# Kernel tuning notes

Measured on AMD Instinct MI355X. Metric: run time of the kernel, lower is better.

## Reference

```python
import jax, jax.numpy as jnp
import numpy as np

EMBED_DIM = 1024
CONTEXT_DIM = 768
NUM_HEADS = 16
HEAD_DIM = EMBED_DIM // NUM_HEADS
B, N, M = 8, 4096, 77


def setup_inputs() -> dict:
    key = jax.random.key(0)
    ks = jax.random.split(key, 12)
    s_in = 1.0 / np.sqrt(EMBED_DIM)
    s_ctx = 1.0 / np.sqrt(CONTEXT_DIM)
    x = jax.random.normal(ks[0], (B, N, EMBED_DIM), dtype=jnp.float32)
    context = jax.random.normal(ks[1], (B, M, CONTEXT_DIM), dtype=jnp.float32)
    # realistic padding mask: each example has a random valid prefix length in [1, M]
    lengths = jax.random.randint(ks[2], (B,), 1, M + 1)
    context_mask = jnp.arange(M)[None, :] < lengths[:, None]  # (B, M) bool
    Wq = jax.random.uniform(ks[3], (EMBED_DIM, EMBED_DIM), jnp.float32, -s_in, s_in)
    bq = jax.random.uniform(ks[4], (EMBED_DIM,), jnp.float32, -s_in, s_in)
    Wk = jax.random.uniform(ks[5], (CONTEXT_DIM, EMBED_DIM), jnp.float32, -s_ctx, s_ctx)
    bk = jax.random.uniform(ks[6], (EMBED_DIM,), jnp.float32, -s_ctx, s_ctx)
    Wv = jax.random.uniform(ks[7], (CONTEXT_DIM, EMBED_DIM), jnp.float32, -s_ctx, s_ctx)
    bv = jax.random.uniform(ks[8], (EMBED_DIM,), jnp.float32, -s_ctx, s_ctx)
    Wo = jax.random.uniform(ks[9], (EMBED_DIM, EMBED_DIM), jnp.float32, -s_in, s_in)
    bo = jax.random.uniform(ks[10], (EMBED_DIM,), jnp.float32, -s_in, s_in)
    return {"x": x, "context": context, "context_mask": context_mask,
            "Wq": Wq, "bq": bq, "Wk": Wk, "bk": bk, "Wv": Wv, "bv": bv,
            "Wo": Wo, "bo": bo}


def reference(x, context, context_mask, Wq, bq, Wk, bk, Wv, bv, Wo, bo):
    H, d = NUM_HEADS, HEAD_DIM
    scale = d ** -0.5
    Bx, Nx, _ = x.shape
    Mx = context.shape[1]
    # projections
    q = (x @ Wq + bq).reshape(Bx, Nx, H, d).transpose(0, 2, 1, 3)        # (B,H,N,d)
    k = (context @ Wk + bk).reshape(Bx, Mx, H, d).transpose(0, 2, 1, 3)  # (B,H,M,d)
    v = (context @ Wv + bv).reshape(Bx, Mx, H, d).transpose(0, 2, 1, 3)  # (B,H,M,d)
    # scores with padding mask
    attn = jnp.einsum('bhnd,bhmd->bhnm', q, k) * scale                   # (B,H,N,M)
    attn = jnp.where(context_mask[:, None, None, :], attn, -jnp.inf)
    attn = jax.nn.softmax(attn, axis=-1)
    out = jnp.einsum('bhnm,bhmd->bhnd', attn, v)                          # (B,H,N,d)
    out = out.transpose(0, 2, 1, 3).reshape(Bx, Nx, H * d)                # (B,N,E)
    return out @ Wo + bo
```

## Files before the change

### kernel.cpp

```cpp
#include <hip/hip_runtime.h>

typedef __bf16 bf16x8 __attribute__((ext_vector_type(8)));
typedef float f32x4 __attribute__((ext_vector_type(4)));

#define EMB 1024
#define CTXD 768
#define NH 16
#define HD 64
#define BB 8
#define NN 4096
#define MM 77
#define MPAD 96

static __device__ __forceinline__ unsigned short f2bf(float f) {
    unsigned u = __builtin_bit_cast(unsigned, f);
    u += 0x7FFFu + ((u >> 16) & 1u);
    return (unsigned short)(u >> 16);
}

struct PrepArgs {
    const float* wsrc[4];
    unsigned short* wdst[4];
    const float* ctx;
    unsigned short* cbf;
    const unsigned char* mask;
    int* lengths;
    int4* kvzero;
    const float* x;
    unsigned short* xbf;
};
__global__ void prep_kernel(PrepArgs pa) {
    const int z = blockIdx.z;
    const int tx = threadIdx.x, ty = threadIdx.y;
    const int tid = ty * 32 + tx;
    if (z < 4) {
        __shared__ float t[32][33];
        int R = (z < 2) ? 1024 : 768, C = 1024;
        int r0 = blockIdx.y * 32;
        if (r0 >= R) return;
        const float* W = pa.wsrc[z];
        unsigned short* Wt = pa.wdst[z];
        int c0 = blockIdx.x * 32;
#pragma unroll
        for (int i = 0; i < 32; i += 8)
            t[ty + i][tx] = W[(size_t)(r0 + ty + i) * C + c0 + tx];
        __syncthreads();
#pragma unroll
        for (int i = 0; i < 32; i += 8)
            Wt[(size_t)(c0 + ty + i) * R + r0 + tx] = f2bf(t[tx][ty + i]);
    } else if (z == 4) {
        int fid = blockIdx.y * 32 + blockIdx.x;
        int i = fid * 256 + tid;
        if (i >= 640 * CTXD / 8) return;
        int row = (i * 8) / CTXD;
        union { unsigned short u[8]; int4 v; } r;
        if (row < BB * MM) {
            float4 v0 = ((const float4*)pa.ctx)[2 * i];
            float4 v1 = ((const float4*)pa.ctx)[2 * i + 1];
            r.u[0] = f2bf(v0.x); r.u[1] = f2bf(v0.y);
            r.u[2] = f2bf(v0.z); r.u[3] = f2bf(v0.w);
            r.u[4] = f2bf(v1.x); r.u[5] = f2bf(v1.y);
            r.u[6] = f2bf(v1.z); r.u[7] = f2bf(v1.w);
        } else {
            r.v = make_int4(0, 0, 0, 0);
        }
        ((int4*)pa.cbf)[i] = r.v;
    } else if (z == 5) {
        int fid = blockIdx.y * 32 + blockIdx.x;
        int i = fid * 256 + tid;
        if (i < 196608) pa.kvzero[i] = make_int4(0, 0, 0, 0);
        if (fid == 1023 && tid < 64) {
            int ln = tid;
            int anyOdd = 0, anyF = 0;
            for (int k = ln; k < BB * MM; k += 64) {
                unsigned char v = pa.mask[k];
                if (v == 0x80u || v == 0x3Fu) anyF = 1;
                if ((k & 3) && v) anyOdd = 1;
            }
            anyF = __any(anyF); anyOdd = __any(anyOdd);
            int layout = anyF ? 2 : (anyOdd ? 1 : 0);
            int b = ln >> 3, j = ln & 7, cnt = 0;
            for (int m = j; m < MM; m += 8) {
                int idx = b * MM + m;
                int valid;
                if (layout == 1)      valid = pa.mask[idx] != 0;
                else if (layout == 0) valid = ((const int*)pa.mask)[idx] != 0;
                else                  valid = ((const float*)pa.mask)[idx] != 0.0f;
                cnt += valid ? 1 : 0;
            }
            cnt += __shfl_xor(cnt, 1, 64);
            cnt += __shfl_xor(cnt, 2, 64);
            cnt += __shfl_xor(cnt, 4, 64);
            if (j == 0) pa.lengths[b] = cnt;
        }
    } else {
        int i = ((z - 6) * 1024 + blockIdx.y * 32 + blockIdx.x) * 256 + tid;
        float4 v0 = ((const float4*)pa.x)[2 * i];
        float4 v1 = ((const float4*)pa.x)[2 * i + 1];
        union { unsigned short u[8]; int4 v; } r;
        r.u[0] = f2bf(v0.x); r.u[1] = f2bf(v0.y);
        r.u[2] = f2bf(v0.z); r.u[3] = f2bf(v0.w);
        r.u[4] = f2bf(v1.x); r.u[5] = f2bf(v1.y);
        r.u[6] = f2bf(v1.z); r.u[7] = f2bf(v1.w);
        ((int4*)pa.xbf)[i] = r.v;
    }
}

__global__ __launch_bounds__(512, 2) void gemm_q_kv(
    const unsigned short* __restrict__ Xbf, const unsigned short* __restrict__ Wq_t,
    const float* __restrict__ bq, unsigned short* __restrict__ Qb,
    const unsigned short* __restrict__ Cbf,
    const unsigned short* __restrict__ Wk_t, const float* __restrict__ bk,
    unsigned short* __restrict__ Kw,
    const unsigned short* __restrict__ Wv_t, const float* __restrict__ bv,
    unsigned short* __restrict__ Vtw) {
    __shared__ unsigned short lds[4][2][256 * 32];
    const int tid = threadIdx.x, wv = tid >> 6, ln = tid & 63;
    int bid = blockIdx.x;

    if (bid < 80) {
        const bool isV = bid >= 40;
        if (isV) bid -= 40;
        const unsigned short* Bt = isV ? Wv_t : Wk_t;
        const float* bias = isV ? bv : bk;
        { int cpx = 5; bid = (bid & 7) * cpx + (bid >> 3); }
        const int nt = bid & 7, mt = bid >> 3;
        const int m0 = mt << 7, n0 = nt << 7;
        const int wr = wv >> 2, wc = wv & 3;
        unsigned short* As = &lds[0][0][0];
        unsigned short* Bs = &lds[0][1][0];

        f32x4 acc[4][2] = {};
        const int rown = ln >> 2, koff = (ln & 3) * 8;
        for (int kt = 0; kt < CTXD; kt += 32) {
            __syncthreads();
            __builtin_amdgcn_global_load_lds(
                (const __attribute__((address_space(1))) void*)(
                    Cbf + (size_t)(m0 + wv * 16 + rown) * CTXD + kt + koff),
                (__attribute__((address_space(3))) void*)(As + wv * 512),
                16, 0, 0);
            __builtin_amdgcn_global_load_lds(
                (const __attribute__((address_space(1))) void*)(
                    Bt + (size_t)(n0 + wv * 16 + rown) * CTXD + kt + koff),
                (__attribute__((address_space(3))) void*)(Bs + wv * 512),
                16, 0, 0);
            __syncthreads();
            bf16x8 af[4], bfr[2];
#pragma unroll
            for (int i = 0; i < 4; ++i)
                af[i] = *(const bf16x8*)(As + (wr * 64 + i * 16 + (ln & 15)) * 32 +
                                         (ln >> 4) * 8);
#pragma unroll
            for (int j = 0; j < 2; ++j)
                bfr[j] = *(const bf16x8*)(Bs + (wc * 32 + j * 16 + (ln & 15)) * 32 +
                                          (ln >> 4) * 8);
#pragma unroll
            for (int i = 0; i < 4; ++i)
#pragma unroll
                for (int j = 0; j < 2; ++j)
                    acc[i][j] = __builtin_amdgcn_mfma_f32_16x16x32_bf16(
                        af[i], bfr[j], acc[i][j], 0, 0, 0);
        }

        float bvals[2];
#pragma unroll
        for (int j = 0; j < 2; ++j)
            bvals[j] = bias[n0 + wc * 32 + j * 16 + (ln & 15)];
#pragma unroll
        for (int i = 0; i < 4; ++i)
#pragma unroll
            for (int j = 0; j < 2; ++j)
#pragma unroll
                for (int r = 0; r < 4; ++r) {
                    int row = m0 + wr * 64 + i * 16 + (ln >> 4) * 4 + r;
                    int col = n0 + wc * 32 + j * 16 + (ln & 15);
                    float v = acc[i][j][r] + bvals[j];
                    if (row < BB * MM) {
                        int bb = row / MM, m = row - bb * MM;
                        int hh = col >> 6, d = col & 63;
                        if (!isV)
                            Kw[((size_t)(bb * NH + hh) * MPAD + m) * HD + d] = f2bf(v);
                        else
                            Vtw[((size_t)(bb * NH + hh) * HD + d) * MPAD + m] = f2bf(v);
                    }
                }
        return;
    }

    bid -= 80;
    const int M = 32768, N = 1024, K = 1024;
    const int numN = N >> 8;
    const int nwg = (M >> 8) * numN;
    { int cpx = nwg >> 3; bid = (bid & 7) * cpx + (bid >> 3); }
    const int nt_ = bid % numN, mt = bid / numN;
    const int m0 = mt << 8, n0 = nt_ << 8;
    const int wr = wv >> 2, wc = wv & 3;
    const int NT = K >> 5;

    const int srow = wv * 16 + (ln >> 2);
    const int sslot = ln & 3;

    auto stageA = [&](int t) {
#pragma unroll
        for (int half = 0; half < 2; ++half) {
            int row = half * 128 + srow;
            int gc = sslot ^ ((row >> 1) & 3);
            __builtin_amdgcn_global_load_lds(
                (const __attribute__((address_space(1))) void*)(
                    Xbf + (size_t)(m0 + row) * K + (t << 5) + gc * 8),
                (__attribute__((address_space(3))) void*)(
                    &lds[t & 3][0][(half * 128 + wv * 16) * 32]),
                16, 0, 0);
        }
    };
    auto stageB = [&](int t) {
#pragma unroll
        for (int half = 0; half < 2; ++half) {
            int row = half * 128 + srow;
            int gc = sslot ^ ((row >> 1) & 3);
            __builtin_amdgcn_global_load_lds(
                (const __attribute__((address_space(1))) void*)(
                    Wq_t + (size_t)(n0 + row) * K + (t << 5) + gc * 8),
                (__attribute__((address_space(3))) void*)(
                    &lds[t & 3][1][(half * 128 + wv * 16) * 32]),
                16, 0, 0);
        }
    };
    auto readA = [&](const unsigned short* As, int i) -> bf16x8 {
        int arow = wr * 128 + i * 16 + (ln & 15);
        int aslot = (ln >> 4) ^ ((arow >> 1) & 3);
        return *(const bf16x8*)(As + arow * 32 + aslot * 8);
    };
    auto readB = [&](const unsigned short* Bs, int j) -> bf16x8 {
        int brow = wc * 64 + j * 16 + (ln & 15);
        int bslot = (ln >> 4) ^ ((brow >> 1) & 3);
        return *(const bf16x8*)(Bs + brow * 32 + bslot * 8);
    };

    f32x4 acc[8][4] = {};

    stageA(0); stageB(0); stageA(1); stageB(1); stageA(2); stageB(2);
    asm volatile("s_waitcnt vmcnt(8)" ::: "memory");
    __builtin_amdgcn_sched_barrier(0);
    __builtin_amdgcn_s_barrier();

#pragma unroll 4
    for (int t = 0; t < NT; ++t) {
        const unsigned short* As = lds[t & 3][0];
        const unsigned short* Bs = lds[t & 3][1];
        if (t + 3 < NT) stageA(t + 3);
        bf16x8 bfr[4], af[4];
#pragma unroll
        for (int j = 0; j < 4; ++j) bfr[j] = readB(Bs, j);
#pragma unroll
        for (int i = 0; i < 4; ++i) af[i] = readA(As, i);
        __builtin_amdgcn_s_barrier();
        __builtin_amdgcn_s_setprio(1);
#pragma unroll
        for (int i = 0; i < 4; ++i)
#pragma unroll
            for (int j = 0; j < 4; ++j)
                acc[i][j] = __builtin_amdgcn_mfma_f32_16x16x32_bf16(
                    af[i], bfr[j], acc[i][j], 0, 0, 0);
        __builtin_amdgcn_s_setprio(0);
        __builtin_amdgcn_s_barrier();
        if (t + 3 < NT) stageB(t + 3);
#pragma unroll
        for (int i = 0; i < 4; ++i) af[i] = readA(As, i + 4);
        __builtin_amdgcn_s_barrier();
        __builtin_amdgcn_s_setprio(1);
#pragma unroll
        for (int i = 0; i < 4; ++i)
#pragma unroll
            for (int j = 0; j < 4; ++j)
                acc[i + 4][j] = __builtin_amdgcn_mfma_f32_16x16x32_bf16(
                    af[i], bfr[j], acc[i + 4][j], 0, 0, 0);
        __builtin_amdgcn_s_setprio(0);
        if (t < NT - 1) {
            if (t + 3 < NT)      { asm volatile("s_waitcnt vmcnt(4)" ::: "memory"); }
            else if (t + 2 < NT) { asm volatile("s_waitcnt vmcnt(2)" ::: "memory"); }
            else                 { asm volatile("s_waitcnt vmcnt(0)" ::: "memory"); }
            __builtin_amdgcn_sched_barrier(0);
        }
        __builtin_amdgcn_s_barrier();
    }

    float bvals[4];
#pragma unroll
    for (int j = 0; j < 4; ++j)
        bvals[j] = bq[n0 + wc * 64 + j * 16 + (ln & 15)];
#pragma unroll
    for (int i = 0; i < 8; ++i)
#pragma unroll
        for (int j = 0; j < 4; ++j)
#pragma unroll
            for (int r = 0; r < 4; ++r) {
                int row = m0 + wr * 128 + i * 16 + (ln >> 4) * 4 + r;
                int col = n0 + wc * 64 + j * 16 + (ln & 15);
                Qb[(size_t)row * N + col] = f2bf(acc[i][j][r] + bvals[j]);
            }
}

__global__ __launch_bounds__(512, 2) void gemm256_kernel(
    const unsigned short* __restrict__ A, const unsigned short* __restrict__ Bt,
    const float* __restrict__ bias, float* __restrict__ Cout,
    int M, int N, int K) {
    __shared__ unsigned short lds[4][2][256 * 32];
    const int tid = threadIdx.x, wv = tid >> 6, ln = tid & 63;
    const int numN = N >> 8;
    int bid = blockIdx.x;
    const int nwg = (M >> 8) * numN;
    if ((nwg & 7) == 0) { int cpx = nwg >> 3; bid = (bid & 7) * cpx + (bid >> 3); }
    const int nt_ = bid % numN, mt = bid / numN;
    const int m0 = mt << 8, n0 = nt_ << 8;
    const int wr = wv >> 2, wc = wv & 3;
    const int NT = K >> 5;

    const int srow = wv * 16 + (ln >> 2);
    const int sslot = ln & 3;

    auto stageA = [&](int t) {
#pragma unroll
        for (int half = 0; half < 2; ++half) {
            int row = half * 128 + srow;
            int gc = sslot ^ ((row >> 1) & 3);
            __builtin_amdgcn_global_load_lds(
                (const __attribute__((address_space(1))) void*)(
                    A + (size_t)(m0 + row) * K + (t << 5) + gc * 8),
                (__attribute__((address_space(3))) void*)(
                    &lds[t & 3][0][(half * 128 + wv * 16) * 32]),
                16, 0, 0);
        }
    };
    auto stageB = [&](int t) {
#pragma unroll
        for (int half = 0; half < 2; ++half) {
            int row = half * 128 + srow;
            int gc = sslot ^ ((row >> 1) & 3);
            __builtin_amdgcn_global_load_lds(
                (const __attribute__((address_space(1))) void*)(
                    Bt + (size_t)(n0 + row) * K + (t << 5) + gc * 8),
                (__attribute__((address_space(3))) void*)(
                    &lds[t & 3][1][(half * 128 + wv * 16) * 32]),
                16, 0, 0);
        }
    };
    auto readA = [&](const unsigned short* As, int i) -> bf16x8 {
        int arow = wr * 128 + i * 16 + (ln & 15);
        int aslot = (ln >> 4) ^ ((arow >> 1) & 3);
        return *(const bf16x8*)(As + arow * 32 + aslot * 8);
    };
    auto readB = [&](const unsigned short* Bs, int j) -> bf16x8 {
        int brow = wc * 64 + j * 16 + (ln & 15);
        int bslot = (ln >> 4) ^ ((brow >> 1) & 3);
        return *(const bf16x8*)(Bs + brow * 32 + bslot * 8);
    };

    f32x4 acc[8][4] = {};

    stageA(0); stageB(0); stageA(1); stageB(1); stageA(2); stageB(2);
    asm volatile("s_waitcnt vmcnt(8)" ::: "memory");
    __builtin_amdgcn_sched_barrier(0);
    __builtin_amdgcn_s_barrier();

#pragma unroll 4
    for (int t = 0; t < NT; ++t) {
        const unsigned short* As = lds[t & 3][0];
        const unsigned short* Bs = lds[t & 3][1];
        if (t + 3 < NT) stageA(t + 3);
        bf16x8 bfr[4], af[4];
#pragma unroll
        for (int j = 0; j < 4; ++j) bfr[j] = readB(Bs, j);
#pragma unroll
        for (int i = 0; i < 4; ++i) af[i] = readA(As, i);
        __builtin_amdgcn_s_barrier();
        __builtin_amdgcn_s_setprio(1);
#pragma unroll
        for (int i = 0; i < 4; ++i)
#pragma unroll
            for (int j = 0; j < 4; ++j)
                acc[i][j] = __builtin_amdgcn_mfma_f32_16x16x32_bf16(
                    af[i], bfr[j], acc[i][j], 0, 0, 0);
        __builtin_amdgcn_s_setprio(0);
        __builtin_amdgcn_s_barrier();
        if (t + 3 < NT) stageB(t + 3);
#pragma unroll
        for (int i = 0; i < 4; ++i) af[i] = readA(As, i + 4);
        __builtin_amdgcn_s_barrier();
        __builtin_amdgcn_s_setprio(1);
#pragma unroll
        for (int i = 0; i < 4; ++i)
#pragma unroll
            for (int j = 0; j < 4; ++j)
                acc[i + 4][j] = __builtin_amdgcn_mfma_f32_16x16x32_bf16(
                    af[i], bfr[j], acc[i + 4][j], 0, 0, 0);
        __builtin_amdgcn_s_setprio(0);
        if (t < NT - 1) {
            if (t + 3 < NT)      { asm volatile("s_waitcnt vmcnt(4)" ::: "memory"); }
            else if (t + 2 < NT) { asm volatile("s_waitcnt vmcnt(2)" ::: "memory"); }
            else                 { asm volatile("s_waitcnt vmcnt(0)" ::: "memory"); }
            __builtin_amdgcn_sched_barrier(0);
        }
        __builtin_amdgcn_s_barrier();
    }

    float bvals[4];
#pragma unroll
    for (int j = 0; j < 4; ++j)
        bvals[j] = bias[n0 + wc * 64 + j * 16 + (ln & 15)];
#pragma unroll
    for (int i = 0; i < 8; ++i)
#pragma unroll
        for (int j = 0; j < 4; ++j)
#pragma unroll
            for (int r = 0; r < 4; ++r) {
                int row = m0 + wr * 128 + i * 16 + (ln >> 4) * 4 + r;
                int col = n0 + wc * 64 + j * 16 + (ln & 15);
                Cout[(size_t)row * N + col] = acc[i][j][r] + bvals[j];
            }
}

__global__ __launch_bounds__(256, 3) void attn_kernel(
    const unsigned short* __restrict__ Q, const unsigned short* __restrict__ Kw,
    const unsigned short* __restrict__ Vt, const int* __restrict__ lengths,
    unsigned short* __restrict__ Out) {
    const int bh = blockIdx.y;
    const int b = bh >> 4, h = bh & 15;
    const int q0 = blockIdx.x * 128;
    const int tid = threadIdx.x, wv = tid >> 6, ln = tid & 63;
    const int len = lengths[b];
    const int kscnt = (len + 31) >> 5;

    __shared__ unsigned short Ps[128][104];

    const unsigned short* Ksrc = Kw + (size_t)bh * (MPAD * HD);
    const unsigned short* Vsrc = Vt + (size_t)bh * (HD * MPAD);

    bf16x8 aq[2][2];
#pragma unroll
    for (int qi = 0; qi < 2; ++qi) {
        const int qr = q0 + wv * 32 + qi * 16 + (ln & 15);
        const unsigned short* qptr =
            Q + (size_t)(b * NN + qr) * EMB + h * HD + (ln >> 4) * 8;
        aq[qi][0] = *(const bf16x8*)(qptr);
        aq[qi][1] = *(const bf16x8*)(qptr + 32);
    }

    bf16x8 vf[3][4];
#pragma unroll
    for (int j = 0; j < 4; ++j)
        vf[0][j] = *(const bf16x8*)(Vsrc + (j * 16 + (ln & 15)) * MPAD +
                                    (ln >> 4) * 8);
    if (kscnt > 1) {
#pragma unroll
        for (int j = 0; j < 4; ++j)
            vf[1][j] = *(const bf16x8*)(Vsrc + (j * 16 + (ln & 15)) * MPAD + 32 +
                                        (ln >> 4) * 8);
    }
    if (kscnt > 2) {
#pragma unroll
        for (int j = 0; j < 4; ++j)
            vf[2][j] = *(const bf16x8*)(Vsrc + (j * 16 + (ln & 15)) * MPAD + 64 +
                                        (ln >> 4) * 8);
    }

    f32x4 s[2][5] = {};
#pragma unroll
    for (int t = 0; t < 5; ++t) {
        if (t * 16 < len) {
            const unsigned short* kp =
                Ksrc + (t * 16 + (ln & 15)) * HD + (ln >> 4) * 8;
            bf16x8 k0 = *(const bf16x8*)(kp);
            bf16x8 k1 = *(const bf16x8*)(kp + 32);
#pragma unroll
            for (int qi = 0; qi < 2; ++qi) {
                s[qi][t] = __builtin_amdgcn_mfma_f32_16x16x32_bf16(
                    aq[qi][0], k0, s[qi][t], 0, 0, 0);
                s[qi][t] = __builtin_amdgcn_mfma_f32_16x16x32_bf16(
                    aq[qi][1], k1, s[qi][t], 0, 0, 0);
            }
        }
    }

    const float scale = 0.125f;
    float mx[2][4], sum[2][4];
#pragma unroll
    for (int qi = 0; qi < 2; ++qi)
#pragma unroll
        for (int r = 0; r < 4; ++r) { mx[qi][r] = -1e30f; sum[qi][r] = 0.f; }
#pragma unroll
    for (int t = 0; t < 5; ++t) {
        int m = t * 16 + (ln & 15);
        bool valid = m < len;
#pragma unroll
        for (int qi = 0; qi < 2; ++qi)
#pragma unroll
            for (int r = 0; r < 4; ++r) {
                float v = valid ? s[qi][t][r] * scale : -1e30f;
                s[qi][t][r] = v;
                mx[qi][r] = fmaxf(mx[qi][r], v);
            }
    }
#pragma unroll
    for (int d = 1; d < 16; d <<= 1)
#pragma unroll
        for (int qi = 0; qi < 2; ++qi)
#pragma unroll
            for (int r = 0; r < 4; ++r)
                mx[qi][r] = fmaxf(mx[qi][r], __shfl_xor(mx[qi][r], d, 64));
#pragma unroll
    for (int t = 0; t < 5; ++t)
#pragma unroll
        for (int qi = 0; qi < 2; ++qi)
#pragma unroll
            for (int r = 0; r < 4; ++r) {
                float p = __expf(s[qi][t][r] - mx[qi][r]);
                s[qi][t][r] = p;
                sum[qi][r] += p;
            }
#pragma unroll
    for (int d = 1; d < 16; d <<= 1)
#pragma unroll
        for (int qi = 0; qi < 2; ++qi)
#pragma unroll
            for (int r = 0; r < 4; ++r)
                sum[qi][r] += __shfl_xor(sum[qi][r], d, 64);

    float rinv[2][4];
#pragma unroll
    for (int qi = 0; qi < 2; ++qi)
#pragma unroll
        for (int r = 0; r < 4; ++r) rinv[qi][r] = 1.0f / sum[qi][r];

#pragma unroll
    for (int t = 0; t < 6; ++t)
#pragma unroll
        for (int qi = 0; qi < 2; ++qi)
#pragma unroll
            for (int r = 0; r < 4; ++r) {
                int row = wv * 32 + qi * 16 + (ln >> 4) * 4 + r;
                float v = (t < 5) ? s[qi][t][r] * rinv[qi][r] : 0.0f;
                Ps[row][t * 16 + (ln & 15)] = f2bf(v);
            }

    f32x4 o[2][4] = {};
    for (int ks = 0; ks < kscnt; ++ks) {
#pragma unroll
        for (int qi = 0; qi < 2; ++qi) {
            bf16x8 pf = *(const bf16x8*)(&Ps[wv * 32 + qi * 16 + (ln & 15)]
                                            [ks * 32 + (ln >> 4) * 8]);
#pragma unroll
            for (int j = 0; j < 4; ++j)
                o[qi][j] = __builtin_amdgcn_mfma_f32_16x16x32_bf16(
                    vf[ks][j], pf, o[qi][j], 0, 0, 0);
        }
    }

#pragma unroll
    for (int qi = 0; qi < 2; ++qi) {
        const int qrow = q0 + wv * 32 + qi * 16 + (ln & 15);
        unsigned short* obase =
            Out + (size_t)(b * NN + qrow) * EMB + h * HD + (ln >> 4) * 4;
#pragma unroll
        for (int j = 0; j < 4; ++j) {
            union { unsigned short u[4]; unsigned long long ll; } pk;
#pragma unroll
            for (int r = 0; r < 4; ++r) pk.u[r] = f2bf(o[qi][j][r]);
            *(unsigned long long*)(obase + j * 16) = pk.ll;
        }
    }
}

extern "C" void kernel_launch(void* const* d_in, const int* in_sizes, int n_in,
                              void* d_out, int out_size, void* d_ws, size_t ws_size,
                              hipStream_t stream) {
    const float* x    = (const float*)d_in[0];
    const float* ctx  = (const float*)d_in[1];
    const unsigned char* cmask = (const unsigned char*)d_in[2];
    const float* Wq = (const float*)d_in[3];
    const float* bq = (const float*)d_in[4];
    const float* Wk = (const float*)d_in[5];
    const float* bk = (const float*)d_in[6];
    const float* Wv = (const float*)d_in[7];
    const float* bv = (const float*)d_in[8];
    const float* Wo = (const float*)d_in[9];
    const float* bo = (const float*)d_in[10];

    char* ws = (char*)d_ws;
    unsigned short* Xbf   = (unsigned short*)(ws);
    unsigned short* Wq_t  = (unsigned short*)(ws + 67108864);
    unsigned short* Wo_t  = (unsigned short*)(ws + 69206016);
    unsigned short* Wk_t  = (unsigned short*)(ws + 71303168);
    unsigned short* Wv_t  = (unsigned short*)(ws + 72876032);
    unsigned short* Cbf   = (unsigned short*)(ws + 74448896);
    unsigned short* Kw    = (unsigned short*)(ws + 75431936);
    unsigned short* Vtw   = (unsigned short*)(ws + 77004800);
    int* lengths          = (int*)(ws + 78577664);
    unsigned short* Qb    = (unsigned short*)d_out;

    PrepArgs pa;
    pa.wsrc[0] = Wq; pa.wsrc[1] = Wo; pa.wsrc[2] = Wk; pa.wsrc[3] = Wv;
    pa.wdst[0] = Wq_t; pa.wdst[1] = Wo_t; pa.wdst[2] = Wk_t; pa.wdst[3] = Wv_t;
    pa.ctx = ctx; pa.cbf = Cbf; pa.mask = cmask; pa.lengths = lengths;
    pa.kvzero = (int4*)Kw;
    pa.x = x; pa.xbf = Xbf;
    prep_kernel<<<dim3(32, 32, 22), dim3(32, 8), 0, stream>>>(pa);

    gemm_q_kv<<<592, 512, 0, stream>>>(Xbf, Wq_t, bq, Qb,
                                       Cbf, Wk_t, bk, Kw, Wv_t, bv, Vtw);

    attn_kernel<<<dim3(32, 128), 256, 0, stream>>>(Qb, Kw, Vtw, lengths, Xbf);

    gemm256_kernel<<<512, 512, 0, stream>>>(Xbf, Wo_t, bo, (float*)d_out,
                                            32768, 1024, 1024);
}
```

Baseline: 265.0 us.

## Fuse fp32-to-bf16 conversion of x into the Q projection GEMM

Drops the separate prep pass that converts x to bf16. The Q GEMM now streams fp32 x tiles straight into LDS with an XOR swizzle and converts to bf16 when it reads fragments for the MFMAs. This removes a full write and re-read of a bf16 copy of x. In exchange it adds conversion ALU work inside the hot loop, repeated for each column-wave. The A tile is twice as large in LDS, so the pipeline shrinks from 4 stages to 3 buffers with prefetch distance 2.

```diff
diff --git a/kernel.cpp b/kernel.cpp
--- a/kernel.cpp
+++ b/kernel.cpp
@@ -26,8 +26,6 @@
     const unsigned char* mask;
     int* lengths;
     int4* kvzero;
-    const float* x;
-    unsigned short* xbf;
 };
 __global__ void prep_kernel(PrepArgs pa) {
     const int z = blockIdx.z;
@@ -65,7 +63,7 @@
             r.v = make_int4(0, 0, 0, 0);
         }
         ((int4*)pa.cbf)[i] = r.v;
-    } else if (z == 5) {
+    } else {
         int fid = blockIdx.y * 32 + blockIdx.x;
         int i = fid * 256 + tid;
         if (i < 196608) pa.kvzero[i] = make_int4(0, 0, 0, 0);
@@ -93,28 +91,18 @@
             cnt += __shfl_xor(cnt, 4, 64);
             if (j == 0) pa.lengths[b] = cnt;
         }
-    } else {
-        int i = ((z - 6) * 1024 + blockIdx.y * 32 + blockIdx.x) * 256 + tid;
-        float4 v0 = ((const float4*)pa.x)[2 * i];
-        float4 v1 = ((const float4*)pa.x)[2 * i + 1];
-        union { unsigned short u[8]; int4 v; } r;
-        r.u[0] = f2bf(v0.x); r.u[1] = f2bf(v0.y);
-        r.u[2] = f2bf(v0.z); r.u[3] = f2bf(v0.w);
-        r.u[4] = f2bf(v1.x); r.u[5] = f2bf(v1.y);
-        r.u[6] = f2bf(v1.z); r.u[7] = f2bf(v1.w);
-        ((int4*)pa.xbf)[i] = r.v;
     }
 }
 
 __global__ __launch_bounds__(512, 2) void gemm_q_kv(
-    const unsigned short* __restrict__ Xbf, const unsigned short* __restrict__ Wq_t,
+    const float* __restrict__ X, const unsigned short* __restrict__ Wq_t,
     const float* __restrict__ bq, unsigned short* __restrict__ Qb,
     const unsigned short* __restrict__ Cbf,
     const unsigned short* __restrict__ Wk_t, const float* __restrict__ bk,
     unsigned short* __restrict__ Kw,
     const unsigned short* __restrict__ Wv_t, const float* __restrict__ bv,
     unsigned short* __restrict__ Vtw) {
-    __shared__ unsigned short lds[4][2][256 * 32];
+    __shared__ char smem[147456];
     const int tid = threadIdx.x, wv = tid >> 6, ln = tid & 63;
     int bid = blockIdx.x;
 
@@ -127,8 +115,8 @@
         const int nt = bid & 7, mt = bid >> 3;
         const int m0 = mt << 7, n0 = nt << 7;
         const int wr = wv >> 2, wc = wv & 3;
-        unsigned short* As = &lds[0][0][0];
-        unsigned short* Bs = &lds[0][1][0];
+        unsigned short* As = (unsigned short*)smem;
+        unsigned short* Bs = (unsigned short*)(smem + 8192);
 
         f32x4 acc[4][2] = {};
         const int rown = ln >> 2, koff = (ln & 3) * 8;
@@ -188,72 +176,85 @@
     }
 
     bid -= 80;
-    const int M = 32768, N = 1024, K = 1024;
-    const int numN = N >> 8;
-    const int nwg = (M >> 8) * numN;
+    const int N = 1024, K = 1024;
+    const int nwg = 128 * 4;
     { int cpx = nwg >> 3; bid = (bid & 7) * cpx + (bid >> 3); }
-    const int nt_ = bid % numN, mt = bid / numN;
+    const int nt_ = bid & 3, mt = bid >> 2;
     const int m0 = mt << 8, n0 = nt_ << 8;
     const int wr = wv >> 2, wc = wv & 3;
     const int NT = K >> 5;
 
-    const int srow = wv * 16 + (ln >> 2);
-    const int sslot = ln & 3;
-
-    auto stageA = [&](int t) {
+    const int srowB = wv * 16 + (ln >> 2);
+    const int sslotB = ln & 3;
+    const int arowS = wv * 8 + (ln >> 3);
+    const int aslotS = ln & 7;
+
+    auto stageA = [&](int t, int buf) {
+#pragma unroll
+        for (int half = 0; half < 2; ++half)
+#pragma unroll
+            for (int sub = 0; sub < 2; ++sub) {
+                int row = half * 128 + sub * 64 + arowS;
+                int cs = aslotS ^ (row & 7);
+                __builtin_amdgcn_global_load_lds(
+                    (const __attribute__((address_space(1))) void*)(
+                        X + (size_t)(m0 + row) * K + (t << 5) + cs * 4),
+                    (__attribute__((address_space(3))) void*)(
+                        smem + buf * 32768 +
+                        (half * 128 + sub * 64 + wv * 8) * 128),
+                    16, 0, 0);
+            }
+    };
+    auto stageB = [&](int t, int buf) {
 #pragma unroll
         for (int half = 0; half < 2; ++half) {
-            int row = half * 128 + srow;
-            int gc = sslot ^ ((row >> 1) & 3);
-            __builtin_amdgcn_global_load_lds(
-                (const __attribute__((address_space(1))) void*)(
-                    Xbf + (size_t)(m0 + row) * K + (t << 5) + gc * 8),
-                (__attribute__((address_space(3))) void*)(
-                    &lds[t & 3][0][(half * 128 + wv * 16) * 32]),
-                16, 0, 0);
-        }
-    };
-    auto stageB = [&](int t) {
-#pragma unroll
-        for (int half = 0; half < 2; ++half) {
-            int row = half * 128 + srow;
-            int gc = sslot ^ ((row >> 1) & 3);
+            int row = half * 128 + srowB;
+            int gc = sslotB ^ ((row >> 1) & 3);
             __builtin_amdgcn_global_load_lds(
                 (const __attribute__((address_space(1))) void*)(
                     Wq_t + (size_t)(n0 + row) * K + (t << 5) + gc * 8),
                 (__attribute__((address_space(3))) void*)(
-                    &lds[t & 3][1][(half * 128 + wv * 16) * 32]),
+                    smem + 98304 + buf * 16384 +
+                    (half * 128 + wv * 16) * 64),
                 16, 0, 0);
         }
     };
-    auto readA = [&](const unsigned short* As, int i) -> bf16x8 {
+    auto readA = [&](int buf, int i) -> bf16x8 {
         int arow = wr * 128 + i * 16 + (ln & 15);
-        int aslot = (ln >> 4) ^ ((arow >> 1) & 3);
-        return *(const bf16x8*)(As + arow * 32 + aslot * 8);
-    };
-    auto readB = [&](const unsigned short* Bs, int j) -> bf16x8 {
+        int g = ln >> 4;
+        int sA = (2 * g) ^ (arow & 7);
+        const float* Af = (const float*)(smem + buf * 32768) + arow * 32;
+        f32x4 lo = *(const f32x4*)(Af + sA * 4);
+        f32x4 hi = *(const f32x4*)(Af + (sA ^ 1) * 4);
+        union { unsigned short u[8]; bf16x8 v; } r;
+        r.u[0] = f2bf(lo[0]); r.u[1] = f2bf(lo[1]);
+        r.u[2] = f2bf(lo[2]); r.u[3] = f2bf(lo[3]);
+        r.u[4] = f2bf(hi[0]); r.u[5] = f2bf(hi[1]);
+        r.u[6] = f2bf(hi[2]); r.u[7] = f2bf(hi[3]);
+        return r.v;
+    };
+    auto readB = [&](int buf, int j) -> bf16x8 {
         int brow = wc * 64 + j * 16 + (ln & 15);
         int bslot = (ln >> 4) ^ ((brow >> 1) & 3);
+        const unsigned short* Bs = (const unsigned short*)(smem + 98304 + buf * 16384);
         return *(const bf16x8*)(Bs + brow * 32 + bslot * 8);
     };
 
     f32x4 acc[8][4] = {};
 
-    stageA(0); stageB(0); stageA(1); stageB(1); stageA(2); stageB(2);
-    asm volatile("s_waitcnt vmcnt(8)" ::: "memory");
+    stageA(0, 0); stageB(0, 0); stageA(1, 1); stageB(1, 1);
+    asm volatile("s_waitcnt vmcnt(6)" ::: "memory");
     __builtin_amdgcn_sched_barrier(0);
     __builtin_amdgcn_s_barrier();
 
-#pragma unroll 4
-    for (int t = 0; t < NT; ++t) {
-        const unsigned short* As = lds[t & 3][0];
-        const unsigned short* Bs = lds[t & 3][1];
-        if (t + 3 < NT) stageA(t + 3);
+    auto body = [&](int t, int cur, int tgt) {
+        if (t >= NT) return;
+        if (t + 2 < NT) stageA(t + 2, tgt);
         bf16x8 bfr[4], af[4];
 #pragma unroll
-        for (int j = 0; j < 4; ++j) bfr[j] = readB(Bs, j);
-#pragma unroll
-        for (int i = 0; i < 4; ++i) af[i] = readA(As, i);
+        for (int j = 0; j < 4; ++j) bfr[j] = readB(cur, j);
+#pragma unroll
+        for (int i = 0; i < 4; ++i) af[i] = readA(cur, i);
         __builtin_amdgcn_s_barrier();
         __builtin_amdgcn_s_setprio(1);
 #pragma unroll
@@ -264,9 +265,9 @@
                     af[i], bfr[j], acc[i][j], 0, 0, 0);
         __builtin_amdgcn_s_setprio(0);
         __builtin_amdgcn_s_barrier();
-        if (t + 3 < NT) stageB(t + 3);
-#pragma unroll
-        for (int i = 0; i < 4; ++i) af[i] = readA(As, i + 4);
+        if (t + 2 < NT) stageB(t + 2, tgt);
+#pragma unroll
+        for (int i = 0; i < 4; ++i) af[i] = readA(cur, i + 4);
         __builtin_amdgcn_s_barrier();
         __builtin_amdgcn_s_setprio(1);
 #pragma unroll
@@ -276,13 +277,16 @@
                 acc[i + 4][j] = __builtin_amdgcn_mfma_f32_16x16x32_bf16(
                     af[i], bfr[j], acc[i + 4][j], 0, 0, 0);
         __builtin_amdgcn_s_setprio(0);
-        if (t < NT - 1) {
-            if (t + 3 < NT)      { asm volatile("s_waitcnt vmcnt(4)" ::: "memory"); }
-            else if (t + 2 < NT) { asm volatile("s_waitcnt vmcnt(2)" ::: "memory"); }
-            else                 { asm volatile("s_waitcnt vmcnt(0)" ::: "memory"); }
-            __builtin_amdgcn_sched_barrier(0);
-        }
-        __builtin_amdgcn_s_barrier();
+        if (t + 2 < NT)      { asm volatile("s_waitcnt vmcnt(6)" ::: "memory"); }
+        else if (t + 1 < NT) { asm volatile("s_waitcnt vmcnt(0)" ::: "memory"); }
+        __builtin_amdgcn_sched_barrier(0);
+        __builtin_amdgcn_s_barrier();
+    };
+
+    for (int tb = 0; tb < NT; tb += 3) {
+        body(tb + 0, 0, 2);
+        body(tb + 1, 1, 0);
+        body(tb + 2, 2, 1);
     }
 
     float bvals[4];
@@ -603,10 +607,9 @@
     pa.wdst[0] = Wq_t; pa.wdst[1] = Wo_t; pa.wdst[2] = Wk_t; pa.wdst[3] = Wv_t;
     pa.ctx = ctx; pa.cbf = Cbf; pa.mask = cmask; pa.lengths = lengths;
     pa.kvzero = (int4*)Kw;
-    pa.x = x; pa.xbf = Xbf;
-    prep_kernel<<<dim3(32, 32, 22), dim3(32, 8), 0, stream>>>(pa);
-
-    gemm_q_kv<<<592, 512, 0, stream>>>(Xbf, Wq_t, bq, Qb,
+    prep_kernel<<<dim3(32, 32, 6), dim3(32, 8), 0, stream>>>(pa);
+
+    gemm_q_kv<<<592, 512, 0, stream>>>(x, Wq_t, bq, Qb,
                                        Cbf, Wk_t, bk, Kw, Wv_t, bv, Vtw);
 
     attn_kernel<<<dim3(32, 128), 256, 0, stream>>>(Qb, Kw, Vtw, lengths, Xbf);
```

After: 292.5 us. 1.1x slower.
